# Kernel tuning notes

Measured on AMD Instinct MI355X. Metric: run time of the kernel, lower is better.

## Reference

```python
import jax, jax.numpy as jnp
import numpy as np

N_TOKENS = 8192
TOP_K = 2
N_EXPERTS = 8
D_IN = 2048
D_OUT = 2048


def setup_inputs() -> dict:
    key = jax.random.key(0)
    k1, k2, k3, k4 = jax.random.split(key, 4)
    inputs = jax.random.normal(k1, (N_TOKENS, D_IN), dtype=jnp.float32)
    # stored as [E, out, in], matching nn.Parameter(torch.empty(E, output_size, input_size))
    expert_weights = 0.02 * jax.random.normal(k2, (N_EXPERTS, D_OUT, D_IN), dtype=jnp.float32)
    gates = jax.nn.softmax(jax.random.normal(k3, (N_TOKENS, TOP_K), dtype=jnp.float32), axis=-1)
    # per (token, slot) expert assignment, then sort by expert as the router would
    flat_experts = jax.random.randint(k4, (N_TOKENS * TOP_K,), 0, N_EXPERTS, dtype=jnp.int32)
    sorted_scattered_idxs = jnp.argsort(flat_experts).astype(jnp.int32)
    sorted_expert_idxs = flat_experts[sorted_scattered_idxs]
    expert_offsets = jnp.cumsum(jnp.bincount(flat_experts, length=N_EXPERTS)).astype(jnp.int32)
    return {
        "inputs": inputs,
        "expert_weights": expert_weights,
        "gates": gates,
        "k": TOP_K,
        "sorted_expert_idxs": sorted_expert_idxs,
        "sorted_scattered_idxs": sorted_scattered_idxs,
        "expert_offsets": expert_offsets,
    }


def reference(inputs, expert_weights, gates, k, sorted_expert_idxs, sorted_scattered_idxs, expert_offsets):
    N, d_in = inputs.shape
    E = expert_weights.shape[0]
    Nk = N * k
    # forward permutes weight [E, out, in] -> [E, in, out]
    W = jnp.transpose(expert_weights, (0, 2, 1))
    d_out = W.shape[-1]
    # invert the sort: expert id for each flat (token, slot) index
    expert_per_flat = jnp.zeros((Nk,), dtype=sorted_expert_idxs.dtype).at[
        sorted_scattered_idxs].set(sorted_expert_idxs)
    # scatter2scatter: out_flat[j] = x[j // k] @ W[expert_per_flat[j]]
    x_rep = jnp.repeat(inputs, k, axis=0)  # [N*k, d_in]
    out_flat = jnp.zeros((Nk, d_out), dtype=inputs.dtype)
    for e in range(E):  # small fixed expert count; masked grouped GEMM
        mask = (expert_per_flat == e)[:, None]
        out_flat = out_flat + jnp.where(mask, x_rep, 0.0) @ W[e]
    # combine: (gates.unsqueeze(1) @ output_expanded).squeeze(1)
    out = jnp.einsum('nk,nkd->nd', gates, out_flat.reshape(N, k, d_out))
    return out
```

## Files before the change

kernel.cpp:

```cpp
#include <hip/hip_runtime.h>
#include <hip/hip_bf16.h>
#include <stdint.h>

#define NTOK   8192
#define TOPK   2
#define NEXP   8
#define DIN    2048
#define DOUT   2048
#define NK     (NTOK*TOPK)

typedef __bf16 bf16_8 __attribute__((ext_vector_type(8)));
typedef float  f32x4  __attribute__((ext_vector_type(4)));

__device__ __forceinline__ void gl2lds16(const void* g, void* l) {
  auto gp = reinterpret_cast<const __attribute__((address_space(1))) uint32_t*>(
      reinterpret_cast<uintptr_t>(g));
  auto lp = reinterpret_cast<__attribute__((address_space(3))) uint32_t*>(
      reinterpret_cast<uintptr_t>(l));
  __builtin_amdgcn_global_load_lds(gp, lp, 16, 0, 0);
}

__global__ void cvt_all(const float4* __restrict__ w, uint4* __restrict__ wD,
                        const float4* __restrict__ x, uint4* __restrict__ xD,
                        int nW) {
  int b = blockIdx.x;
  const float4* src;
  uint4* dst;
  int i;
  if (b < nW) { src = w; dst = wD; i = b * 256 + threadIdx.x; }
  else        { src = x; dst = xD; i = (b - nW) * 256 + threadIdx.x; }
  float4 a0 = src[2 * i];
  float4 a1 = src[2 * i + 1];
  union { __bf16 h[8]; uint4 u; } r;
  r.h[0] = (__bf16)a0.x; r.h[1] = (__bf16)a0.y; r.h[2] = (__bf16)a0.z; r.h[3] = (__bf16)a0.w;
  r.h[4] = (__bf16)a1.x; r.h[5] = (__bf16)a1.y; r.h[6] = (__bf16)a1.z; r.h[7] = (__bf16)a1.w;
  dst[i] = r.u;
}

__global__ __launch_bounds__(256, 4)
void moe_gemm(const __bf16* __restrict__ X,
              const __bf16* __restrict__ W,
              const int* __restrict__ ssi,
              const int* __restrict__ offs,
              __bf16* __restrict__ flat)
{
  __shared__ __bf16 lA[2][128 * 32];
  __shared__ __bf16 lB[2][128 * 32];
  __shared__ int   sTok[128];
  __shared__ int   sF[128];

  const int tid = threadIdx.x;
  const int bid = blockIdx.x;
  const int nt  = bid & 15;
  const int mtg = bid >> 4;

  int start = 0, end = 0, e, cum = 0, prev = 0, mloc = 0, found = 0;
  for (e = 0; e < NEXP; ++e) {
    int oe  = offs[e];
    int seg = oe - prev;
    int t   = (seg + 127) >> 7;
    if (mtg < cum + t) { start = prev; end = oe; mloc = mtg - cum; found = 1; break; }
    cum += t; prev = oe;
  }
  if (!found) return;

  const int m0 = start + mloc * 128;

  if (tid < 128) {
    int p     = m0 + tid;
    int valid = p < end;
    int f     = ssi[valid ? p : (end - 1)];
    sTok[tid] = f >> 1;
    sF[tid]   = valid ? f : -1;
  }
  __syncthreads();

  const int rs = tid >> 2;
  const int kc = tid & 3;
  const __bf16* pA0 = X + (size_t)sTok[rs]      * DIN + kc * 8;
  const __bf16* pA1 = X + (size_t)sTok[rs + 64] * DIN + kc * 8;
  const __bf16* wB  = W + (size_t)e * DOUT * DIN + (size_t)(nt * 128) * DIN;
  const __bf16* pB0 = wB + (size_t)rs        * DIN + kc * 8;
  const __bf16* pB1 = wB + (size_t)(rs + 64) * DIN + kc * 8;
  char* ldsAb = (char*)lA + (tid & 192) * 16;
  char* ldsBb = (char*)lB + (tid & 192) * 16;

  const int w  = tid >> 6;
  const int l  = tid & 63;
  const int wm = w >> 1, wn = w & 1;
  const int lr = l & 15;
  const int kq = l >> 4;
  const __bf16* aBase = (const __bf16*)lA + (wm * 64 + lr) * 32 + kq * 8;
  const __bf16* bBase = (const __bf16*)lB + (wn * 64 + lr) * 32 + kq * 8;

  gl2lds16(pA0, ldsAb);
  gl2lds16(pA1, ldsAb + 4096);
  gl2lds16(pB0, ldsBb);
  gl2lds16(pB1, ldsBb + 4096);
  pA0 += 32; pA1 += 32; pB0 += 32; pB1 += 32;

  f32x4 acc[4][4] = {};

  for (int it = 0; it < DIN / 32; ++it) {
    const int cur = it & 1;
    __syncthreads();
    if (it < DIN / 32 - 1) {
      const int nb = cur ^ 1;
      char* a = ldsAb + nb * 8192;
      char* b = ldsBb + nb * 8192;
      gl2lds16(pA0, a);
      gl2lds16(pA1, a + 4096);
      gl2lds16(pB0, b);
      gl2lds16(pB1, b + 4096);
      pA0 += 32; pA1 += 32; pB0 += 32; pB1 += 32;
    }

    const __bf16* aB = aBase + cur * 4096;
    const __bf16* bB = bBase + cur * 4096;
    bf16_8 af[4], bf[4];
#pragma unroll
    for (int am = 0; am < 4; ++am) af[am] = *(const bf16_8*)(aB + am * 512);
#pragma unroll
    for (int bn = 0; bn < 4; ++bn) bf[bn] = *(const bf16_8*)(bB + bn * 512);
#pragma unroll
    for (int am = 0; am < 4; ++am)
#pragma unroll
      for (int bn = 0; bn < 4; ++bn)
        acc[am][bn] = __builtin_amdgcn_mfma_f32_16x16x32_bf16(
            af[am], bf[bn], acc[am][bn], 0, 0, 0);
  }

  const int colBase = nt * 128 + wn * 64 + lr;
  const int rq = kq * 4;
#pragma unroll
  for (int am = 0; am < 4; ++am) {
#pragma unroll
    for (int v = 0; v < 4; ++v) {
      int rl = wm * 64 + am * 16 + rq + v;
      int f  = sF[rl];
      if (f < 0) continue;
      __bf16* row = flat + (size_t)f * DOUT + colBase;
#pragma unroll
      for (int bn = 0; bn < 4; ++bn)
        row[bn * 16] = (__bf16)acc[am][bn][v];
    }
  }
}

__global__ __launch_bounds__(256)
void combine(const __bf16* __restrict__ flat, const float* __restrict__ gates,
             float* __restrict__ out) {
  const int n = blockIdx.x;
  const int c = threadIdx.x * 8;
  bf16_8 y0 = *(const bf16_8*)(flat + (size_t)(2 * n)     * DOUT + c);
  bf16_8 y1 = *(const bf16_8*)(flat + (size_t)(2 * n + 1) * DOUT + c);
  const float2 g = *(const float2*)(gates + 2 * n);
  float o[8];
#pragma unroll
  for (int j = 0; j < 8; ++j)
    o[j] = g.x * (float)y0[j] + g.y * (float)y1[j];
  float4* dst = (float4*)(out + (size_t)n * DOUT + c);
  dst[0] = *(float4*)&o[0];
  dst[1] = *(float4*)&o[4];
}

extern "C" void kernel_launch(void* const* d_in, const int* in_sizes, int n_in,
                              void* d_out, int out_size, void* d_ws, size_t ws_size,
                              hipStream_t stream) {
  const float* inputs = (const float*)d_in[0];
  const float* ew     = (const float*)d_in[1];
  const float* gates  = (const float*)d_in[2];
  const int*   ssi    = (const int*)d_in[5];
  const int*   offs   = (const int*)d_in[6];
  float* out = (float*)d_out;

  __bf16* wsW = (__bf16*)d_ws;
  __bf16* wsX = wsW + (size_t)NEXP * DOUT * DIN;
  __bf16* wsF = wsX + (size_t)NTOK * DIN;

  const int n8w = NEXP * DOUT * DIN / 8;
  const int n8x = NTOK * DIN / 8;
  const int nWb = n8w / 256, nXb = n8x / 256;
  cvt_all<<<nWb + nXb, 256, 0, stream>>>((const float4*)ew, (uint4*)wsW,
                                         (const float4*)inputs, (uint4*)wsX, nWb);

  moe_gemm<<<136 * 16, 256, 0, stream>>>(wsX, wsW, ssi, offs, wsF);
  combine<<<NTOK, 256, 0, stream>>>(wsF, gates, out);
}
```

Measured before the change: 454.8 us.

## Enlarge MoE GEMM tile to 256x128 with 512 threads and XOR-swizzled LDS

Raises the per-block M tile from 128 to 256 rows and uses 8 waves per block, so each weight tile loaded into LDS is reused across twice as many token rows. It also XOR-swizzles the k-chunk position in LDS on both the global-to-LDS writes and the fragment reads, to cut bank conflicts. The cost is more padding waste per expert segment, fewer blocks in the grid, and more LDS per block, which can lower occupancy.

```diff
diff --git a/kernel.cpp b/kernel.cpp
--- a/kernel.cpp
+++ b/kernel.cpp
@@ -8,6 +8,10 @@
 #define DIN    2048
 #define DOUT   2048
 #define NK     (NTOK*TOPK)
+
+#define BM 256
+#define BN 128
+#define BK 32
 
 typedef __bf16 bf16_8 __attribute__((ext_vector_type(8)));
 typedef float  f32x4  __attribute__((ext_vector_type(4)));
@@ -37,17 +41,17 @@
   dst[i] = r.u;
 }
 
-__global__ __launch_bounds__(256, 4)
+__global__ __launch_bounds__(512, 4)
 void moe_gemm(const __bf16* __restrict__ X,
               const __bf16* __restrict__ W,
               const int* __restrict__ ssi,
               const int* __restrict__ offs,
               __bf16* __restrict__ flat)
 {
-  __shared__ __bf16 lA[2][128 * 32];
-  __shared__ __bf16 lB[2][128 * 32];
-  __shared__ int   sTok[128];
-  __shared__ int   sF[128];
+  __shared__ __bf16 lA[2][BM * BK];
+  __shared__ __bf16 lB[2][BN * BK];
+  __shared__ int   sTok[BM];
+  __shared__ int   sF[BM];
 
   const int tid = threadIdx.x;
   const int bid = blockIdx.x;
@@ -58,15 +62,15 @@
   for (e = 0; e < NEXP; ++e) {
     int oe  = offs[e];
     int seg = oe - prev;
-    int t   = (seg + 127) >> 7;
+    int t   = (seg + BM - 1) >> 8;
     if (mtg < cum + t) { start = prev; end = oe; mloc = mtg - cum; found = 1; break; }
     cum += t; prev = oe;
   }
   if (!found) return;
 
-  const int m0 = start + mloc * 128;
+  const int m0 = start + mloc * BM;
 
-  if (tid < 128) {
+  if (tid < BM) {
     int p     = m0 + tid;
     int valid = p < end;
     int f     = ssi[valid ? p : (end - 1)];
@@ -76,47 +80,43 @@
   __syncthreads();
 
   const int rs = tid >> 2;
-  const int kc = tid & 3;
-  const __bf16* pA0 = X + (size_t)sTok[rs]      * DIN + kc * 8;
-  const __bf16* pA1 = X + (size_t)sTok[rs + 64] * DIN + kc * 8;
-  const __bf16* wB  = W + (size_t)e * DOUT * DIN + (size_t)(nt * 128) * DIN;
-  const __bf16* pB0 = wB + (size_t)rs        * DIN + kc * 8;
-  const __bf16* pB1 = wB + (size_t)(rs + 64) * DIN + kc * 8;
-  char* ldsAb = (char*)lA + (tid & 192) * 16;
-  char* ldsBb = (char*)lB + (tid & 192) * 16;
+  const int kc = (tid & 3) ^ ((tid >> 3) & 3);
+  const __bf16* pA0 = X + (size_t)sTok[rs]       * DIN + kc * 8;
+  const __bf16* pA1 = X + (size_t)sTok[rs + 128] * DIN + kc * 8;
+  const __bf16* wB  = W + (size_t)e * DOUT * DIN + (size_t)(nt * BN) * DIN;
+  const __bf16* pB0 = wB + (size_t)rs * DIN + kc * 8;
+  char* ldsAb = (char*)lA + (tid >> 6) * 1024;
+  char* ldsBb = (char*)lB + (tid >> 6) * 1024;
 
-  const int w  = tid >> 6;
-  const int l  = tid & 63;
-  const int wm = w >> 1, wn = w & 1;
-  const int lr = l & 15;
-  const int kq = l >> 4;
-  const __bf16* aBase = (const __bf16*)lA + (wm * 64 + lr) * 32 + kq * 8;
-  const __bf16* bBase = (const __bf16*)lB + (wn * 64 + lr) * 32 + kq * 8;
+  const int w   = tid >> 6;
+  const int l   = tid & 63;
+  const int wm  = w >> 1, wn = w & 1;
+  const int lr  = l & 15;
+  const int kq  = l >> 4;
+  const int kqs = kq ^ ((lr >> 1) & 3);
+  const __bf16* aBase = (const __bf16*)lA + (wm * 64 + lr) * BK + kqs * 8;
+  const __bf16* bBase = (const __bf16*)lB + (wn * 64 + lr) * BK + kqs * 8;
 
   gl2lds16(pA0, ldsAb);
-  gl2lds16(pA1, ldsAb + 4096);
+  gl2lds16(pA1, ldsAb + 8192);
   gl2lds16(pB0, ldsBb);
-  gl2lds16(pB1, ldsBb + 4096);
-  pA0 += 32; pA1 += 32; pB0 += 32; pB1 += 32;
+  pA0 += BK; pA1 += BK; pB0 += BK;
 
   f32x4 acc[4][4] = {};
 
-  for (int it = 0; it < DIN / 32; ++it) {
+  for (int it = 0; it < DIN / BK; ++it) {
     const int cur = it & 1;
     __syncthreads();
-    if (it < DIN / 32 - 1) {
+    if (it < DIN / BK - 1) {
       const int nb = cur ^ 1;
-      char* a = ldsAb + nb * 8192;
-      char* b = ldsBb + nb * 8192;
-      gl2lds16(pA0, a);
-      gl2lds16(pA1, a + 4096);
-      gl2lds16(pB0, b);
-      gl2lds16(pB1, b + 4096);
-      pA0 += 32; pA1 += 32; pB0 += 32; pB1 += 32;
+      gl2lds16(pA0, ldsAb + nb * 16384);
+      gl2lds16(pA1, ldsAb + nb * 16384 + 8192);
+      gl2lds16(pB0, ldsBb + nb * 8192);
+      pA0 += BK; pA1 += BK; pB0 += BK;
     }
 
-    const __bf16* aB = aBase + cur * 4096;
-    const __bf16* bB = bBase + cur * 4096;
+    const __bf16* aB = aBase + cur * (BM * BK);
+    const __bf16* bB = bBase + cur * (BN * BK);
     bf16_8 af[4], bf[4];
 #pragma unroll
     for (int am = 0; am < 4; ++am) af[am] = *(const bf16_8*)(aB + am * 512);
@@ -130,7 +130,7 @@
             af[am], bf[bn], acc[am][bn], 0, 0, 0);
   }
 
-  const int colBase = nt * 128 + wn * 64 + lr;
+  const int colBase = nt * BN + wn * 64 + lr;
   const int rq = kq * 4;
 #pragma unroll
   for (int am = 0; am < 4; ++am) {
@@ -184,6 +184,6 @@
   cvt_all<<<nWb + nXb, 256, 0, stream>>>((const float4*)ew, (uint4*)wsW,
                                          (const float4*)inputs, (uint4*)wsX, nWb);
 
-  moe_gemm<<<136 * 16, 256, 0, stream>>>(wsX, wsW, ssi, offs, wsF);
+  moe_gemm<<<72 * 16, 512, 0, stream>>>(wsX, wsW, ssi, offs, wsF);
   combine<<<NTOK, 256, 0, stream>>>(wsF, gates, out);
 }
```

Measured after the change: 441.6 us. 2.9% less time.
